# Performance work log

Hardware: AMD Instinct MI355X
Metric: run time of the kernel (lower is better)

Reference implementation:

```python
import jax, jax.numpy as jnp
import numpy as np

S, B, H, V, C = 2048, 64, 300, 50257, 2


def setup_inputs() -> dict:
    key = jax.random.key(0)
    ks = jax.random.split(key, 8)
    x = jax.random.randint(ks[0], (S, B), 0, V)              # token ids, seq-first like nn.RNN default
    emb = jax.random.normal(ks[1], (V, H), jnp.float32) * 0.02
    W_ih = jax.random.normal(ks[2], (H, H), jnp.float32) * (1.0 / np.sqrt(H))
    W_hh = jax.random.normal(ks[3], (H, H), jnp.float32) * (1.0 / np.sqrt(H))
    b_ih = jax.random.normal(ks[4], (H,), jnp.float32) * 0.01
    b_hh = jax.random.normal(ks[5], (H,), jnp.float32) * 0.01
    W_out = jax.random.normal(ks[6], (C, H), jnp.float32) * (1.0 / np.sqrt(H))
    b_out = jnp.zeros((C,), jnp.float32)
    return {"x": x, "emb": emb, "W_ih": W_ih, "W_hh": W_hh,
            "b_ih": b_ih, "b_hh": b_hh, "W_out": W_out, "b_out": b_out}


def reference(x, emb, W_ih, W_hh, b_ih, b_hh, W_out, b_out):
    e = emb[x]                                               # (S, B, H) embedding lookup
    # Precompute input projection for all timesteps (batched GEMM), fold both biases in.
    xp = jnp.einsum('sbh,ih->sbi', e, W_ih) + b_ih + b_hh    # (S, B, H)

    def step(h, xt):
        h = jax.nn.relu(xt + h @ W_hh.T)                     # Elman: relu(W x_t + U h_{t-1} + b)
        return h, h

    h0 = jnp.zeros((B, H), xp.dtype)
    hT, hs = jax.lax.scan(step, h0, xp)                      # hs: (S, B, H)

    y = jax.nn.relu(hs)                                      # faithful to original's extra relu (idempotent)
    pooled = jnp.max(y, axis=1)                              # max over dim=1 (batch in seq-first layout) -> (S, H)
    out = pooled @ W_out.T + b_out                           # (S, C)
    return out, hT[None]                                     # hidden: (1, B, H) like nn.RNN
```

## Files before the change

### kernel.cpp

```cpp
#include <hip/hip_runtime.h>

typedef unsigned short u16;
typedef unsigned int   u32;
typedef unsigned long long u64;
typedef short s16x8 __attribute__((ext_vector_type(8)));
typedef float f32x4 __attribute__((ext_vector_type(4)));
typedef u32   u32x2 __attribute__((ext_vector_type(2)));
typedef _Float16 f16x2 __attribute__((ext_vector_type(2)));

#define S_LEN 2048
#define BATCH 64
#define H_DIM 300
#define HP    304
#define KP    320

#define OFF_WPAD 0u
#define OFF_BIAS 196608u
#define OFF_FLAG 198656u
#define OFF_H    200704u
#define OFF_POOL 278528u
#define OFF_WHH  2768896u
#define OFF_XP   3158016u

__device__ __forceinline__ float bf2f(u16 u){
  union { u32 i; float f; } v; v.i = ((u32)u) << 16; return v.f;
}
__device__ __forceinline__ u16 f2bf(float f){
  u32 i = __float_as_uint(f);
  u32 r = (i + 0x7fffu + ((i >> 16) & 1u)) >> 16;
  return (u16)r;
}
__device__ __forceinline__ f16x2 asH2(u32 u){
  union { u32 u; f16x2 h; } v; v.u = u; return v.h;
}
__device__ __forceinline__ u16 f2h(float f){
  union { _Float16 h; u16 u; } v; v.h = (_Float16)f; return v.u;
}

#if __has_builtin(__builtin_amdgcn_fdot2)
#define FD(WU, HU, C) __builtin_amdgcn_fdot2(asH2(WU), asH2(HU), (C), false)
#else
__device__ __forceinline__ float fd_fb(u32 wu, u32 hu, float c){
  const f16x2 w = asH2(wu), h = asH2(hu);
  c = fmaf((float)w.x, (float)h.x, c);
  c = fmaf((float)w.y, (float)h.y, c);
  return c;
}
#define FD(WU, HU, C) fd_fb((WU), (HU), (C))
#endif

__global__ __launch_bounds__(256) void detect(const u16* __restrict__ emb_raw,
                                              int* __restrict__ flag){
  __shared__ int big;
  if (threadIdx.x == 0) big = 0;
  __syncthreads();
  int loc = 0;
  for (int i = threadIdx.x; i < 1024; i += 256){
    const u32 e = ((u32)emb_raw[i] >> 7) & 0xFFu;
    if (e >= 135u) loc = 1;
  }
  if (loc) atomicOr(&big, 1);
  __syncthreads();
  if (threadIdx.x == 0) *flag = big;
}

__global__ __launch_bounds__(256) void prep(
    const void* __restrict__ Wih_raw, const void* __restrict__ Whh_raw,
    const void* __restrict__ bih_raw, const void* __restrict__ bhh_raw,
    const int* __restrict__ flag,
    u16* __restrict__ Wpad, u32* __restrict__ Whh16,
    float* __restrict__ biasp, float* __restrict__ pooled,
    u32* __restrict__ hstate)
{
  const bool isf32 = (*flag != 0);
  const int idx = blockIdx.x * 256 + threadIdx.x;
  if (idx < S_LEN * HP) pooled[idx] = 0.f;
  if (idx < BATCH * 160) hstate[idx] = 0u;
  if (idx < 320 * 160){
    const int r = idx / 160, j = idx % 160;
    const int k = 2 * j;
    float w0 = 0.f, w1 = 0.f;
    if (r < H_DIM){
      if (k < H_DIM)
        w0 = isf32 ? ((const float*)Whh_raw)[r * H_DIM + k]
                   : bf2f(((const u16*)Whh_raw)[r * H_DIM + k]);
      if (k + 1 < H_DIM)
        w1 = isf32 ? ((const float*)Whh_raw)[r * H_DIM + k + 1]
                   : bf2f(((const u16*)Whh_raw)[r * H_DIM + k + 1]);
    }
    Whh16[idx] = (u32)f2h(w0) | ((u32)f2h(w1) << 16);
  }
  if (idx < HP * KP){
    const int n = idx / KP, k = idx % KP;
    u16 v = 0;
    if (n < H_DIM && k < H_DIM){
      v = isf32 ? f2bf(((const float*)Wih_raw)[n * H_DIM + k])
                : ((const u16*)Wih_raw)[n * H_DIM + k];
    }
    Wpad[idx] = v;
  }
  if (idx < HP){
    float bv = 0.f;
    if (idx < H_DIM){
      bv = isf32 ? (((const float*)bih_raw)[idx] + ((const float*)bhh_raw)[idx])
                 : (bf2f(((const u16*)bih_raw)[idx]) + bf2f(((const u16*)bhh_raw)[idx]));
    }
    biasp[idx] = bv;
  }
}

__global__ __launch_bounds__(256) void xp_gemm(
    const int* __restrict__ x, const void* __restrict__ emb_raw,
    const int* __restrict__ flag,
    const u16* __restrict__ Wpad, const float* __restrict__ biasp,
    float* __restrict__ xp, int s0)
{
  __shared__ u16 A[64 * KP];
  const bool isf32 = (*flag != 0);
  const int tid = threadIdx.x;
  const int m0g = s0 * BATCH + blockIdx.x * 64;
  const int m0r = blockIdx.x * 64;

  for (int t = tid; t < 640; t += 256){
    const int row = t / 10, wd = t % 10;
    *(u32*)&A[row * KP + H_DIM + wd * 2] = 0u;
  }
  for (int t = tid; t < 64 * 75; t += 256){
    const int row = t / 75, off = t % 75;
    const int tok = x[m0g + row];
    u64 pk;
    if (isf32){
      const float4 v = *(const float4*)((const float*)emb_raw + (size_t)tok * H_DIM + off * 4);
      pk = (u64)f2bf(v.x) | ((u64)f2bf(v.y) << 16)
         | ((u64)f2bf(v.z) << 32) | ((u64)f2bf(v.w) << 48);
    } else {
      pk = *(const u64*)((const u16*)emb_raw + (size_t)tok * H_DIM + off * 4);
    }
    *(u64*)&A[row * KP + off * 4] = pk;
  }
  __syncthreads();

  const int wave = tid >> 6, lane = tid & 63;
  const int lm = lane & 15, lq = lane >> 4;

  f32x4 acc[19];
#pragma unroll
  for (int nt = 0; nt < 19; ++nt) acc[nt] = (f32x4){0.f, 0.f, 0.f, 0.f};

#pragma unroll
  for (int ks = 0; ks < 10; ++ks){
    const int k = ks * 32 + lq * 8;
    const s16x8 af = *(const s16x8*)&A[(wave * 16 + lm) * KP + k];
#pragma unroll
    for (int nt = 0; nt < 19; ++nt){
      const s16x8 bf = *(const s16x8*)&Wpad[(nt * 16 + lm) * KP + k];
      acc[nt] = __builtin_amdgcn_mfma_f32_16x16x32_bf16(af, bf, acc[nt], 0, 0, 0);
    }
  }
#pragma unroll
  for (int nt = 0; nt < 19; ++nt){
    const int n = nt * 16 + lm;
    const float bv = biasp[n];
#pragma unroll
    for (int rr = 0; rr < 4; ++rr){
      const int m = m0r + wave * 16 + lq * 4 + rr;
      xp[(size_t)m * HP + n] = acc[nt][rr] + bv;
    }
  }
}

__global__ __launch_bounds__(1024) void recur(
    const float* __restrict__ xp, const u32* __restrict__ Whh16,
    u32* __restrict__ hstate, float* __restrict__ pooled,
    float* __restrict__ dout, int s0, int len)
{
  const int b   = blockIdx.x;
  const int tid = threadIdx.x;
  const int c   = tid >> 6;
  const int l   = tid & 63;
  const int j0  = c * 10;
  const int r0  = l * 4;
  const int r4  = 256 + l;

  __shared__ float part[16 * 320];
  __shared__ u32 hp[160];

  u32x2 qa0,qb0,qc0,qd0,qe0;
  u32x2 qa1,qb1,qc1,qd1,qe1;
  u32x2 qa2,qb2,qc2,qd2,qe2;
  u32x2 qa3,qb3,qc3,qd3,qe3;
  u32x2 qa4,qb4,qc4,qd4,qe4;

#define LOADW(R, ROW) { const u32* wp = Whh16 + (size_t)(ROW) * 160 + j0; \
  qa##R = *(const u32x2*)(wp + 0); qb##R = *(const u32x2*)(wp + 2);       \
  qc##R = *(const u32x2*)(wp + 4); qd##R = *(const u32x2*)(wp + 6);       \
  qe##R = *(const u32x2*)(wp + 8); }
  LOADW(0, r0)
  LOADW(1, r0 + 1)
  LOADW(2, r0 + 2)
  LOADW(3, r0 + 3)
  LOADW(4, r4)
#undef LOADW

  if (tid < 160) hp[tid] = hstate[b * 160 + tid];

  const float* xpb = xp + (size_t)b * HP;
  float xv = 0.f;
  if (tid < 304) xv = xpb[tid];
  __syncthreads();

  for (int t = 0; t < len; ++t){
    float xnext = 0.f;
    if (tid < 304){
      const int tn = (t + 1 < len) ? (t + 1) : t;
      xnext = xpb[(size_t)tn * (BATCH * HP) + tid];
    }
    const u32x2 h0 = *(const u32x2*)&hp[j0 + 0];
    const u32x2 h1 = *(const u32x2*)&hp[j0 + 2];
    const u32x2 h2 = *(const u32x2*)&hp[j0 + 4];
    const u32x2 h3 = *(const u32x2*)&hp[j0 + 6];
    const u32x2 h4 = *(const u32x2*)&hp[j0 + 8];

    float s0v, s1v, s2v, s3v, s4v;
#define DOTROW(R, DST) { float s = 0.f;                              \
    s = FD(qa##R.x, h0.x, s); s = FD(qa##R.y, h0.y, s);              \
    s = FD(qb##R.x, h1.x, s); s = FD(qb##R.y, h1.y, s);              \
    s = FD(qc##R.x, h2.x, s); s = FD(qc##R.y, h2.y, s);              \
    s = FD(qd##R.x, h3.x, s); s = FD(qd##R.y, h3.y, s);              \
    s = FD(qe##R.x, h4.x, s); s = FD(qe##R.y, h4.y, s); DST = s; }
    DOTROW(0, s0v)
    DOTROW(1, s1v)
    DOTROW(2, s2v)
    DOTROW(3, s3v)
    DOTROW(4, s4v)
#undef DOTROW

    *(f32x4*)&part[c * 320 + r0] = (f32x4){s0v, s1v, s2v, s3v};
    part[c * 320 + r4] = s4v;
    __syncthreads();

    if (tid < 304){
      float sum = xv;
#pragma unroll
      for (int cc = 0; cc < 16; ++cc) sum += part[cc * 320 + tid];
      const float h = fmaxf(sum, 0.f);
      const int s = s0 + t;
      if (tid < H_DIM){
        atomicMax((u32*)(pooled + (size_t)s * HP + tid), __float_as_uint(h));
        if (s == S_LEN - 1) dout[S_LEN * 2 + b * H_DIM + tid] = h;
      }
      ((u16*)hp)[tid] = f2h(h);
      xv = xnext;
    }
    __syncthreads();
  }
  if (tid < 160) hstate[b * 160 + tid] = hp[tid];
}

__global__ __launch_bounds__(128) void outproj(
    const float* __restrict__ pooled, const void* __restrict__ Wout_raw,
    const void* __restrict__ bout_raw, const int* __restrict__ flag,
    float* __restrict__ dout)
{
  const bool isf32 = (*flag != 0);
  const int s = blockIdx.x * 128 + threadIdx.x;
  float a0, a1;
  if (isf32){ a0 = ((const float*)bout_raw)[0]; a1 = ((const float*)bout_raw)[1]; }
  else      { a0 = bf2f(((const u16*)bout_raw)[0]); a1 = bf2f(((const u16*)bout_raw)[1]); }
  for (int i = 0; i < H_DIM; ++i){
    const float p = pooled[(size_t)s * HP + i];
    float w0, w1;
    if (isf32){ w0 = ((const float*)Wout_raw)[i]; w1 = ((const float*)Wout_raw)[H_DIM + i]; }
    else      { w0 = bf2f(((const u16*)Wout_raw)[i]); w1 = bf2f(((const u16*)Wout_raw)[H_DIM + i]); }
    a0 = fmaf(p, w0, a0);
    a1 = fmaf(p, w1, a1);
  }
  dout[s * 2 + 0] = a0;
  dout[s * 2 + 1] = a1;
}

extern "C" void kernel_launch(void* const* d_in, const int* in_sizes, int n_in,
                              void* d_out, int out_size, void* d_ws, size_t ws_size,
                              hipStream_t stream)
{
  const int* x  = (const int*)d_in[0];
  const void* emb  = d_in[1];
  const void* Wih  = d_in[2];
  const void* Whh  = d_in[3];
  const void* bih  = d_in[4];
  const void* bhh  = d_in[5];
  const void* Wout = d_in[6];
  const void* bout = d_in[7];
  float* out = (float*)d_out;

  char* ws = (char*)d_ws;
  u16*   Wpad   = (u16*)(ws + OFF_WPAD);
  float* biasp  = (float*)(ws + OFF_BIAS);
  int*   flag   = (int*)(ws + OFF_FLAG);
  u32*   hstate = (u32*)(ws + OFF_H);
  float* pooled = (float*)(ws + OFF_POOL);
  u32*   Whh16  = (u32*)(ws + OFF_WHH);
  float* xp     = (float*)(ws + OFF_XP);

  const size_t per_step = (size_t)BATCH * HP * 4;
  int CH = 16;
  const int cands[8] = {2048, 1024, 512, 256, 128, 64, 32, 16};
  for (int i = 0; i < 8; ++i){
    if ((size_t)OFF_XP + (size_t)cands[i] * per_step <= ws_size){ CH = cands[i]; break; }
  }
  const int nchunks = S_LEN / CH;

  detect<<<1, 256, 0, stream>>>((const u16*)emb, flag);
  prep<<<2432, 256, 0, stream>>>(Wih, Whh, bih, bhh, flag, Wpad, Whh16,
                                 biasp, pooled, hstate);
  for (int k = 0; k < nchunks; ++k){
    const int s0 = k * CH;
    xp_gemm<<<CH, 256, 0, stream>>>(x, emb, flag, Wpad, biasp, xp, s0);
    recur<<<64, 1024, 0, stream>>>(xp, Whh16, hstate, pooled, out, s0, CH);
  }
  outproj<<<16, 128, 0, stream>>>(pooled, Wout, bout, flag, out);
}
```

Measured before the change: 1.883 ms.

## Halve recurrence block size and hold W_hh slices in AGPRs

The recurrence kernel now runs 8 waves per batch element instead of 16, so each wave covers 19 packed columns instead of 10. The larger W_hh slice (95 words per thread) is kept in accumulation registers through inline asm writes and reads. The hidden-state vector in shared memory now uses a padded per-wave stride so each wave can fetch its slice with vector loads. The aim is to halve the cross-wave partial-sum reduction and cut barrier cost per timestep, at the price of a longer serial dot-product chain per wave and an extra register read for every multiply-add.

```diff
diff --git a/kernel.cpp b/kernel.cpp
--- a/kernel.cpp
+++ b/kernel.cpp
@@ -6,6 +6,7 @@
 typedef short s16x8 __attribute__((ext_vector_type(8)));
 typedef float f32x4 __attribute__((ext_vector_type(4)));
 typedef u32   u32x2 __attribute__((ext_vector_type(2)));
+typedef u32   u32x4 __attribute__((ext_vector_type(4)));
 typedef _Float16 f16x2 __attribute__((ext_vector_type(2)));
 
 #define S_LEN 2048
@@ -169,7 +170,12 @@
   }
 }
 
-__global__ __launch_bounds__(1024) void recur(
+#define AWR(A, V) asm volatile("v_accvgpr_write_b32 a" #A ", %0" :: "v"((u32)(V)) : "a" #A)
+#define DOT(A, H, ACC) { u32 wv_; \
+  asm volatile("v_accvgpr_read_b32 %0, a" #A : "=v"(wv_)); \
+  ACC = FD(wv_, (H), ACC); }
+
+__global__ __launch_bounds__(512) void recur(
     const float* __restrict__ xp, const u32* __restrict__ Whh16,
     u32* __restrict__ hstate, float* __restrict__ pooled,
     float* __restrict__ dout, int s0, int len)
@@ -178,31 +184,42 @@
   const int tid = threadIdx.x;
   const int c   = tid >> 6;
   const int l   = tid & 63;
-  const int j0  = c * 10;
+  const int j0  = c * 19;
   const int r0  = l * 4;
   const int r4  = 256 + l;
 
-  __shared__ float part[16 * 320];
-  __shared__ u32 hp[160];
-
-  u32x2 qa0,qb0,qc0,qd0,qe0;
-  u32x2 qa1,qb1,qc1,qd1,qe1;
-  u32x2 qa2,qb2,qc2,qd2,qe2;
-  u32x2 qa3,qb3,qc3,qd3,qe3;
-  u32x2 qa4,qb4,qc4,qd4,qe4;
-
-#define LOADW(R, ROW) { const u32* wp = Whh16 + (size_t)(ROW) * 160 + j0; \
-  qa##R = *(const u32x2*)(wp + 0); qb##R = *(const u32x2*)(wp + 2);       \
-  qc##R = *(const u32x2*)(wp + 4); qd##R = *(const u32x2*)(wp + 6);       \
-  qe##R = *(const u32x2*)(wp + 8); }
-  LOADW(0, r0)
-  LOADW(1, r0 + 1)
-  LOADW(2, r0 + 2)
-  LOADW(3, r0 + 3)
-  LOADW(4, r4)
-#undef LOADW
-
-  if (tid < 160) hp[tid] = hstate[b * 160 + tid];
+  __shared__ float part[8 * 320];
+  __shared__ u32 hq[160];
+
+  {
+    const u32* w0p = Whh16 + (size_t)(r0 + 0) * 160 + j0;
+    AWR(0,w0p[0]);  AWR(1,w0p[1]);  AWR(2,w0p[2]);  AWR(3,w0p[3]);  AWR(4,w0p[4]);
+    AWR(5,w0p[5]);  AWR(6,w0p[6]);  AWR(7,w0p[7]);  AWR(8,w0p[8]);  AWR(9,w0p[9]);
+    AWR(10,w0p[10]);AWR(11,w0p[11]);AWR(12,w0p[12]);AWR(13,w0p[13]);AWR(14,w0p[14]);
+    AWR(15,w0p[15]);AWR(16,w0p[16]);AWR(17,w0p[17]);AWR(18,w0p[18]);
+    const u32* w1p = Whh16 + (size_t)(r0 + 1) * 160 + j0;
+    AWR(19,w1p[0]); AWR(20,w1p[1]); AWR(21,w1p[2]); AWR(22,w1p[3]); AWR(23,w1p[4]);
+    AWR(24,w1p[5]); AWR(25,w1p[6]); AWR(26,w1p[7]); AWR(27,w1p[8]); AWR(28,w1p[9]);
+    AWR(29,w1p[10]);AWR(30,w1p[11]);AWR(31,w1p[12]);AWR(32,w1p[13]);AWR(33,w1p[14]);
+    AWR(34,w1p[15]);AWR(35,w1p[16]);AWR(36,w1p[17]);AWR(37,w1p[18]);
+    const u32* w2p = Whh16 + (size_t)(r0 + 2) * 160 + j0;
+    AWR(38,w2p[0]); AWR(39,w2p[1]); AWR(40,w2p[2]); AWR(41,w2p[3]); AWR(42,w2p[4]);
+    AWR(43,w2p[5]); AWR(44,w2p[6]); AWR(45,w2p[7]); AWR(46,w2p[8]); AWR(47,w2p[9]);
+    AWR(48,w2p[10]);AWR(49,w2p[11]);AWR(50,w2p[12]);AWR(51,w2p[13]);AWR(52,w2p[14]);
+    AWR(53,w2p[15]);AWR(54,w2p[16]);AWR(55,w2p[17]);AWR(56,w2p[18]);
+    const u32* w3p = Whh16 + (size_t)(r0 + 3) * 160 + j0;
+    AWR(57,w3p[0]); AWR(58,w3p[1]); AWR(59,w3p[2]); AWR(60,w3p[3]); AWR(61,w3p[4]);
+    AWR(62,w3p[5]); AWR(63,w3p[6]); AWR(64,w3p[7]); AWR(65,w3p[8]); AWR(66,w3p[9]);
+    AWR(67,w3p[10]);AWR(68,w3p[11]);AWR(69,w3p[12]);AWR(70,w3p[13]);AWR(71,w3p[14]);
+    AWR(72,w3p[15]);AWR(73,w3p[16]);AWR(74,w3p[17]);AWR(75,w3p[18]);
+    const u32* w4p = Whh16 + (size_t)r4 * 160 + j0;
+    AWR(76,w4p[0]); AWR(77,w4p[1]); AWR(78,w4p[2]); AWR(79,w4p[3]); AWR(80,w4p[4]);
+    AWR(81,w4p[5]); AWR(82,w4p[6]); AWR(83,w4p[7]); AWR(84,w4p[8]); AWR(85,w4p[9]);
+    AWR(86,w4p[10]);AWR(87,w4p[11]);AWR(88,w4p[12]);AWR(89,w4p[13]);AWR(90,w4p[14]);
+    AWR(91,w4p[15]);AWR(92,w4p[16]);AWR(93,w4p[17]);AWR(94,w4p[18]);
+  }
+
+  if (tid < 160) hq[tid] = hstate[b * 160 + tid];
 
   const float* xpb = xp + (size_t)b * HP;
   float xv = 0.f;
@@ -215,25 +232,40 @@
       const int tn = (t + 1 < len) ? (t + 1) : t;
       xnext = xpb[(size_t)tn * (BATCH * HP) + tid];
     }
-    const u32x2 h0 = *(const u32x2*)&hp[j0 + 0];
-    const u32x2 h1 = *(const u32x2*)&hp[j0 + 2];
-    const u32x2 h2 = *(const u32x2*)&hp[j0 + 4];
-    const u32x2 h3 = *(const u32x2*)&hp[j0 + 6];
-    const u32x2 h4 = *(const u32x2*)&hp[j0 + 8];
-
-    float s0v, s1v, s2v, s3v, s4v;
-#define DOTROW(R, DST) { float s = 0.f;                              \
-    s = FD(qa##R.x, h0.x, s); s = FD(qa##R.y, h0.y, s);              \
-    s = FD(qb##R.x, h1.x, s); s = FD(qb##R.y, h1.y, s);              \
-    s = FD(qc##R.x, h2.x, s); s = FD(qc##R.y, h2.y, s);              \
-    s = FD(qd##R.x, h3.x, s); s = FD(qd##R.y, h3.y, s);              \
-    s = FD(qe##R.x, h4.x, s); s = FD(qe##R.y, h4.y, s); DST = s; }
-    DOTROW(0, s0v)
-    DOTROW(1, s1v)
-    DOTROW(2, s2v)
-    DOTROW(3, s3v)
-    DOTROW(4, s4v)
-#undef DOTROW
+    const u32* hqc = hq + 20 * c;
+    const u32x4 ha = *(const u32x4*)(hqc + 0);
+    const u32x4 hb = *(const u32x4*)(hqc + 4);
+    const u32x4 hc2 = *(const u32x4*)(hqc + 8);
+    const u32x4 hd = *(const u32x4*)(hqc + 12);
+    const u32x2 he = *(const u32x2*)(hqc + 16);
+    const u32   hf2 = hqc[18];
+
+    float s0v = 0.f, s1v = 0.f, s2v = 0.f, s3v = 0.f, s4v = 0.f;
+    DOT(0,ha.x,s0v)  DOT(1,ha.y,s0v)  DOT(2,ha.z,s0v)  DOT(3,ha.w,s0v)
+    DOT(4,hb.x,s0v)  DOT(5,hb.y,s0v)  DOT(6,hb.z,s0v)  DOT(7,hb.w,s0v)
+    DOT(8,hc2.x,s0v) DOT(9,hc2.y,s0v) DOT(10,hc2.z,s0v)DOT(11,hc2.w,s0v)
+    DOT(12,hd.x,s0v) DOT(13,hd.y,s0v) DOT(14,hd.z,s0v) DOT(15,hd.w,s0v)
+    DOT(16,he.x,s0v) DOT(17,he.y,s0v) DOT(18,hf2,s0v)
+    DOT(19,ha.x,s1v) DOT(20,ha.y,s1v) DOT(21,ha.z,s1v) DOT(22,ha.w,s1v)
+    DOT(23,hb.x,s1v) DOT(24,hb.y,s1v) DOT(25,hb.z,s1v) DOT(26,hb.w,s1v)
+    DOT(27,hc2.x,s1v)DOT(28,hc2.y,s1v)DOT(29,hc2.z,s1v)DOT(30,hc2.w,s1v)
+    DOT(31,hd.x,s1v) DOT(32,hd.y,s1v) DOT(33,hd.z,s1v) DOT(34,hd.w,s1v)
+    DOT(35,he.x,s1v) DOT(36,he.y,s1v) DOT(37,hf2,s1v)
+    DOT(38,ha.x,s2v) DOT(39,ha.y,s2v) DOT(40,ha.z,s2v) DOT(41,ha.w,s2v)
+    DOT(42,hb.x,s2v) DOT(43,hb.y,s2v) DOT(44,hb.z,s2v) DOT(45,hb.w,s2v)
+    DOT(46,hc2.x,s2v)DOT(47,hc2.y,s2v)DOT(48,hc2.z,s2v)DOT(49,hc2.w,s2v)
+    DOT(50,hd.x,s2v) DOT(51,hd.y,s2v) DOT(52,hd.z,s2v) DOT(53,hd.w,s2v)
+    DOT(54,he.x,s2v) DOT(55,he.y,s2v) DOT(56,hf2,s2v)
+    DOT(57,ha.x,s3v) DOT(58,ha.y,s3v) DOT(59,ha.z,s3v) DOT(60,ha.w,s3v)
+    DOT(61,hb.x,s3v) DOT(62,hb.y,s3v) DOT(63,hb.z,s3v) DOT(64,hb.w,s3v)
+    DOT(65,hc2.x,s3v)DOT(66,hc2.y,s3v)DOT(67,hc2.z,s3v)DOT(68,hc2.w,s3v)
+    DOT(69,hd.x,s3v) DOT(70,hd.y,s3v) DOT(71,hd.z,s3v) DOT(72,hd.w,s3v)
+    DOT(73,he.x,s3v) DOT(74,he.y,s3v) DOT(75,hf2,s3v)
+    DOT(76,ha.x,s4v) DOT(77,ha.y,s4v) DOT(78,ha.z,s4v) DOT(79,ha.w,s4v)
+    DOT(80,hb.x,s4v) DOT(81,hb.y,s4v) DOT(82,hb.z,s4v) DOT(83,hb.w,s4v)
+    DOT(84,hc2.x,s4v)DOT(85,hc2.y,s4v)DOT(86,hc2.z,s4v)DOT(87,hc2.w,s4v)
+    DOT(88,hd.x,s4v) DOT(89,hd.y,s4v) DOT(90,hd.z,s4v) DOT(91,hd.w,s4v)
+    DOT(92,he.x,s4v) DOT(93,he.y,s4v) DOT(94,hf2,s4v)
 
     *(f32x4*)&part[c * 320 + r0] = (f32x4){s0v, s1v, s2v, s3v};
     part[c * 320 + r4] = s4v;
@@ -242,19 +274,21 @@
     if (tid < 304){
       float sum = xv;
 #pragma unroll
-      for (int cc = 0; cc < 16; ++cc) sum += part[cc * 320 + tid];
+      for (int cc = 0; cc < 8; ++cc) sum += part[cc * 320 + tid];
       const float h = fmaxf(sum, 0.f);
       const int s = s0 + t;
       if (tid < H_DIM){
         atomicMax((u32*)(pooled + (size_t)s * HP + tid), __float_as_uint(h));
         if (s == S_LEN - 1) dout[S_LEN * 2 + b * H_DIM + tid] = h;
       }
-      ((u16*)hp)[tid] = f2h(h);
+      const int j = tid >> 1;
+      const int w2 = j / 19, p2 = j - w2 * 19;
+      ((u16*)hq)[((w2 * 20 + p2) << 1) | (tid & 1)] = f2h(h);
       xv = xnext;
     }
     __syncthreads();
   }
-  if (tid < 160) hstate[b * 160 + tid] = hp[tid];
+  if (tid < 160) hstate[b * 160 + tid] = hq[tid];
 }
 
 __global__ __launch_bounds__(128) void outproj(
@@ -316,7 +350,7 @@
   for (int k = 0; k < nchunks; ++k){
     const int s0 = k * CH;
     xp_gemm<<<CH, 256, 0, stream>>>(x, emb, flag, Wpad, biasp, xp, s0);
-    recur<<<64, 1024, 0, stream>>>(xp, Whh16, hstate, pooled, out, s0, CH);
+    recur<<<64, 512, 0, stream>>>(xp, Whh16, hstate, pooled, out, s0, CH);
   }
   outproj<<<16, 128, 0, stream>>>(pooled, Wout, bout, flag, out);
 }
```

Result: slower. 2.907 ms (+54.4%).
